# Optimization experiments

Measured on AMD Instinct MI355X. Metric: run time of the kernel, lower is better.

The kernel has to match this reference:

```python
import jax, jax.numpy as jnp
import numpy as np

B, W, V, D, H = 8, 1024, 512, 1024, 8
DK = D // H
SCALE = 1.0 / float(np.sqrt(DK))
EPS = 1e-5


def ln(x, g, b):
    m = x.mean(-1, keepdims=True)
    v = ((x - m) ** 2).mean(-1, keepdims=True)
    return (x - m) * jax.lax.rsqrt(v + EPS) * g + b


def setup_inputs() -> dict:
    key = jax.random.key(0)
    ks = iter(jax.random.split(key, 32))

    def wmat(shape):
        return jax.random.normal(next(ks), shape, jnp.float32) * 0.02

    inp = {
        'x': jax.random.normal(next(ks), (B, W, D), jnp.float32),
        'y': jax.random.normal(next(ks), (B, V, D), jnp.float32),
        'mask': jnp.ones((B, 1, W, W), jnp.bool_),
        # res1 pre-norm
        'ln_r1_g': jnp.ones((D,), jnp.float32), 'ln_r1_b': jnp.zeros((D,), jnp.float32),
        # self-attention projections (stored [in,out])
        'sa_wq': wmat((D, D)), 'sa_bq': jnp.zeros((D,), jnp.float32),
        'sa_wk': wmat((D, D)), 'sa_bk': jnp.zeros((D,), jnp.float32),
        'sa_wv': wmat((D, D)), 'sa_bv': jnp.zeros((D,), jnp.float32),
        'sa_wo': wmat((D, D)), 'sa_bo': jnp.zeros((D,), jnp.float32),
        # cross-attention norms + projections
        'ca_tn_g': jnp.ones((D,), jnp.float32), 'ca_tn_b': jnp.zeros((D,), jnp.float32),
        'ca_an_g': jnp.ones((D,), jnp.float32), 'ca_an_b': jnp.zeros((D,), jnp.float32),
        'ca_wq': wmat((D, D)), 'ca_bq': jnp.zeros((D,), jnp.float32),
        'ca_wk': wmat((D, D)), 'ca_bk': jnp.zeros((D,), jnp.float32),
        'ca_wv': wmat((D, D)), 'ca_bv': jnp.zeros((D,), jnp.float32),
        # post-cross norms
        'n1_g': jnp.ones((D,), jnp.float32), 'n1_b': jnp.zeros((D,), jnp.float32),
        'n2_g': jnp.ones((D,), jnp.float32), 'n2_b': jnp.zeros((D,), jnp.float32),
        # res2 pre-norm + FFN (hidden = 2*D per UniDecoderLayer)
        'ln_r2_g': jnp.ones((D,), jnp.float32), 'ln_r2_b': jnp.zeros((D,), jnp.float32),
        'ff_w1': wmat((D, 2 * D)), 'ff_b1': jnp.zeros((2 * D,), jnp.float32),
        'ff_w2': wmat((2 * D, D)), 'ff_b2': jnp.zeros((D,), jnp.float32),
    }
    return inp


def reference(x, y, mask,
              ln_r1_g, ln_r1_b,
              sa_wq, sa_bq, sa_wk, sa_bk, sa_wv, sa_bv, sa_wo, sa_bo,
              ca_tn_g, ca_tn_b, ca_an_g, ca_an_b,
              ca_wq, ca_bq, ca_wk, ca_bk, ca_wv, ca_bv,
              n1_g, n1_b, n2_g, n2_b,
              ln_r2_g, ln_r2_b, ff_w1, ff_b1, ff_w2, ff_b2):
    # --- res1: x + self_attn(LN(x)) (dropout p=0) ---
    h = ln(x, ln_r1_g, ln_r1_b)
    q = (h @ sa_wq + sa_bq).reshape(B, W, H, DK)
    k = (h @ sa_wk + sa_bk).reshape(B, W, H, DK)
    v = (h @ sa_wv + sa_bv).reshape(B, W, H, DK)
    scores = jnp.einsum('bqhd,bkhd->bhqk', q, k) * SCALE
    scores = jnp.where(mask, scores, jnp.float32(-1e9))  # mask (B,1,W,W) broadcasts over heads
    a = jax.nn.softmax(scores, axis=-1)
    o = jnp.einsum('bhqk,bkhd->bqhd', a, v).reshape(B, W, D)
    x = x + (o @ sa_wo + sa_bo)

    # --- sigmoid-gated cross attention ---
    t = ln(x, ca_tn_g, ca_tn_b)
    av = ln(y, ca_an_g, ca_an_b)
    cq = (t @ ca_wq + ca_bq).reshape(B, W, H, DK)
    ck = (av @ ca_wk + ca_bk).reshape(B, V, H, DK)
    cv = (av @ ca_wv + ca_bv).reshape(B, V, H, DK)
    gate = jax.nn.sigmoid(jnp.einsum('bwhd,bvhd->bwvh', cq, ck) * SCALE)  # (B,W,V,H)
    res = jnp.einsum('bwvh,bvhd->bwhd', gate, cv).reshape(B, W, D)
    attn_out = gate.mean(-1)  # mean over heads -> (B,W,V)

    x = ln(x, n1_g, n1_b) + ln(res, n2_g, n2_b)

    # --- res2: x + FFN(LN(x)) ---
    h2 = ln(x, ln_r2_g, ln_r2_b)
    x = x + (jax.nn.relu(h2 @ ff_w1 + ff_b1) @ ff_w2 + ff_b2)
    return (x, attn_out)
```

## Files before the change

kernel.cpp:

```cpp
#include <hip/hip_runtime.h>


typedef __bf16 bf16;
typedef bf16  bf16x4 __attribute__((ext_vector_type(4)));
typedef bf16  bf16x8 __attribute__((ext_vector_type(8)));
typedef float f32x4  __attribute__((ext_vector_type(4)));

#define SCALE 0.08838834764831845f

__device__ __forceinline__ f32x4 mfma16(bf16x8 a, bf16x8 b, f32x4 c) {
  return __builtin_amdgcn_mfma_f32_16x16x32_bf16(a, b, c, 0, 0, 0);
}

__device__ __forceinline__ void gll16(const bf16* g, bf16* l) {
  __builtin_amdgcn_global_load_lds(
      (__attribute__((address_space(1))) void*)(void*)g,
      (__attribute__((address_space(3))) void*)(void*)l, 16, 0, 0);
}

__device__ __forceinline__ void xcd_tile(int& bm, int& bn) {
  const int nx = gridDim.x;
  const int nwg = nx * gridDim.y;
  int bid = blockIdx.y * nx + blockIdx.x;
  const int cpx = nwg >> 3;
  bid = (bid & 7) * cpx + (bid >> 3);
  bn = (bid % nx) * 128;
  bm = (bid / nx) * 128;
}

__global__ __launch_bounds__(256) void gemm_bt(
    const bf16* __restrict__ A, const bf16* __restrict__ Bt,
    const float* __restrict__ bias,
    const bf16* __restrict__ residB, const float* __restrict__ residF,
    bf16* __restrict__ Cb, float* __restrict__ Cf,
    int M, int N, int K, int relu)
{
  __shared__ alignas(16) bf16 As[128 * 32];
  __shared__ alignas(16) bf16 Bs[128 * 32];
  const int tid  = threadIdx.x;
  const int wid  = tid >> 6;
  const int lane = tid & 63;
  const int l15  = lane & 15;
  const int quad = lane >> 4;
  int bm, bn;
  xcd_tile(bm, bn);
  const int wm = (wid & 1) * 64,  wn = (wid >> 1) * 64;

  f32x4 acc[4][4] = {};

  const int srow = tid >> 2;
  const int scol = (tid & 3) * 8;
  const bf16* ag0 = A  + (long)(bm + srow) * K + scol;
  const bf16* ag1 = ag0 + (long)64 * K;
  const bf16* bg0 = Bt + (long)(bn + srow) * K + scol;
  const bf16* bg1 = bg0 + (long)64 * K;
  bf16* lA0 = As + wid * 512;
  bf16* lA1 = As + 2048 + wid * 512;
  bf16* lB0 = Bs + wid * 512;
  bf16* lB1 = Bs + 2048 + wid * 512;

  for (int k0 = 0; k0 < K; k0 += 32) {
    gll16(ag0 + k0, lA0);
    gll16(ag1 + k0, lA1);
    gll16(bg0 + k0, lB0);
    gll16(bg1 + k0, lB1);
    __syncthreads();
    bf16x8 af[4], bfr[4];
#pragma unroll
    for (int i = 0; i < 4; ++i)
      af[i] = *(const bf16x8*)(As + (wm + i * 16 + l15) * 32 + quad * 8);
#pragma unroll
    for (int i = 0; i < 4; ++i)
      bfr[i] = *(const bf16x8*)(Bs + (wn + i * 16 + l15) * 32 + quad * 8);
#pragma unroll
    for (int mt = 0; mt < 4; ++mt)
#pragma unroll
      for (int nt = 0; nt < 4; ++nt)
        acc[mt][nt] = mfma16(af[mt], bfr[nt], acc[mt][nt]);
    __syncthreads();
  }

#pragma unroll
  for (int nt = 0; nt < 4; ++nt) {
    const int col = bn + wn + nt * 16 + l15;
    const float bv = bias ? bias[col] : 0.f;
#pragma unroll
    for (int mt = 0; mt < 4; ++mt) {
      const int row0 = bm + wm + mt * 16 + quad * 4;
#pragma unroll
      for (int r = 0; r < 4; ++r) {
        const long idx = (long)(row0 + r) * N + col;
        float v = acc[mt][nt][r] + bv;
        if (relu) v = fmaxf(v, 0.f);
        if (residB) v += (float)residB[idx];
        if (residF) v += residF[idx];
        if (Cb) Cb[idx] = (bf16)v;
        if (Cf) Cf[idx] = v;
      }
    }
  }
}

struct Out3 {
  bf16* o0; bf16* o1; bf16* o2;
  const float* b0; const float* b1; const float* b2;
};

__global__ __launch_bounds__(256) void gemm_bt_split(
    const bf16* __restrict__ A, const bf16* __restrict__ Bt,
    Out3 so, int M, int Ntot, int K)
{
  __shared__ alignas(16) bf16 As[128 * 32];
  __shared__ alignas(16) bf16 Bs[128 * 32];
  const int tid  = threadIdx.x;
  const int wid  = tid >> 6;
  const int lane = tid & 63;
  const int l15  = lane & 15;
  const int quad = lane >> 4;
  int bm, bn;
  xcd_tile(bm, bn);
  const int wm = (wid & 1) * 64,  wn = (wid >> 1) * 64;

  const int ch = bn >> 10;
  bf16* C = (ch == 0) ? so.o0 : (ch == 1 ? so.o1 : so.o2);
  const float* bp = (ch == 0) ? so.b0 : (ch == 1 ? so.b1 : so.b2);

  f32x4 acc[4][4] = {};

  const int srow = tid >> 2;
  const int scol = (tid & 3) * 8;
  const bf16* ag0 = A  + (long)(bm + srow) * K + scol;
  const bf16* ag1 = ag0 + (long)64 * K;
  const bf16* bg0 = Bt + (long)(bn + srow) * K + scol;
  const bf16* bg1 = bg0 + (long)64 * K;
  bf16* lA0 = As + wid * 512;
  bf16* lA1 = As + 2048 + wid * 512;
  bf16* lB0 = Bs + wid * 512;
  bf16* lB1 = Bs + 2048 + wid * 512;

  for (int k0 = 0; k0 < K; k0 += 32) {
    gll16(ag0 + k0, lA0);
    gll16(ag1 + k0, lA1);
    gll16(bg0 + k0, lB0);
    gll16(bg1 + k0, lB1);
    __syncthreads();
    bf16x8 af[4], bfr[4];
#pragma unroll
    for (int i = 0; i < 4; ++i)
      af[i] = *(const bf16x8*)(As + (wm + i * 16 + l15) * 32 + quad * 8);
#pragma unroll
    for (int i = 0; i < 4; ++i)
      bfr[i] = *(const bf16x8*)(Bs + (wn + i * 16 + l15) * 32 + quad * 8);
#pragma unroll
    for (int mt = 0; mt < 4; ++mt)
#pragma unroll
      for (int nt = 0; nt < 4; ++nt)
        acc[mt][nt] = mfma16(af[mt], bfr[nt], acc[mt][nt]);
    __syncthreads();
  }

#pragma unroll
  for (int nt = 0; nt < 4; ++nt) {
    const int col = bn + wn + nt * 16 + l15;
    const int cc  = col & 1023;
    const float bv = bp[cc];
#pragma unroll
    for (int mt = 0; mt < 4; ++mt) {
      const int row0 = bm + wm + mt * 16 + quad * 4;
#pragma unroll
      for (int r = 0; r < 4; ++r)
        C[(long)(row0 + r) * 1024 + cc] = (bf16)(acc[mt][nt][r] + bv);
    }
  }
  (void)M; (void)Ntot;
}

__global__ __launch_bounds__(512) void attn_self(
    const bf16* __restrict__ Q, const bf16* __restrict__ Km,
    const bf16* __restrict__ Vt, bf16* __restrict__ O)
{
  __shared__ alignas(16) bf16 Ks[16384];
  __shared__ alignas(16) bf16 Vs[16384];
  __shared__ alignas(16) bf16 Ps[8192];
  const int tid  = threadIdx.x;
  const int wid  = tid >> 6;
  const int lane = tid & 63;
  const int l15  = lane & 15;
  const int quad = lane >> 4;
  const int b = blockIdx.y >> 3, h = blockIdx.y & 7;
  const int q0 = blockIdx.x * 128;

  const int rdoff = l15 * 32 + (((quad ^ ((l15 >> 1) & 3))) << 3);

  const long qb = ((long)(b * 1024 + q0 + wid * 16 + l15)) * 1024 + h * 128 + quad * 8;
  bf16x8 qf[4];
#pragma unroll
  for (int ks = 0; ks < 4; ++ks) qf[ks] = *(const bf16x8*)(Q + qb + ks * 32);

  f32x4 oacc[8] = {};
  float mrow[4], lrow[4];
#pragma unroll
  for (int r = 0; r < 4; ++r) { mrow[r] = -3.0e38f; lrow[r] = 0.f; }

  const long kbase = (long)(b * 1024) * 1024 + h * 128;
  const long vbase = (long)(b * 8 + h) * 128 * 1024;

  const int srow = tid >> 3;
  const int sc8  = (tid & 7) * 8;

  bf16* pw = Ps + wid * 1024;

  for (int t = 0; t < 8; ++t) {
    const int kv0 = t * 128;
    __syncthreads();
#pragma unroll
    for (int dh = 0; dh < 2; ++dh)
#pragma unroll
      for (int kq = 0; kq < 2; ++kq) {
        const int kv = kq * 64 + srow;
        const int d  = dh * 64 + sc8;
        bf16x8 v = *(const bf16x8*)(Km + kbase + (long)(kv0 + kv) * 1024 + d);
        *(bf16x8*)(Ks + (d >> 5) * 4096 + kv * 32 +
                   (((((d & 31) >> 3) ^ ((kv >> 1) & 3))) << 3)) = v;
      }
#pragma unroll
    for (int kh = 0; kh < 2; ++kh)
#pragma unroll
      for (int dq = 0; dq < 2; ++dq) {
        const int d  = dq * 64 + srow;
        const int kv = kh * 64 + sc8;
        bf16x8 v = *(const bf16x8*)(Vt + vbase + (long)d * 1024 + kv0 + kv);
        *(bf16x8*)(Vs + (kv >> 5) * 4096 + d * 32 +
                   (((((kv & 31) >> 3) ^ ((d >> 1) & 3))) << 3)) = v;
      }
    __syncthreads();

    f32x4 sacc[8] = {};
#pragma unroll
    for (int nt = 0; nt < 8; ++nt)
#pragma unroll
      for (int ks = 0; ks < 4; ++ks)
        sacc[nt] = mfma16(qf[ks],
            *(const bf16x8*)(Ks + ks * 4096 + nt * 512 + rdoff),
            sacc[nt]);

    float tm[4];
#pragma unroll
    for (int r = 0; r < 4; ++r) {
      float m = -3.0e38f;
#pragma unroll
      for (int nt = 0; nt < 8; ++nt) m = fmaxf(m, sacc[nt][r]);
      tm[r] = m * SCALE;
    }
#pragma unroll
    for (int off = 8; off; off >>= 1)
#pragma unroll
      for (int r = 0; r < 4; ++r) tm[r] = fmaxf(tm[r], __shfl_xor(tm[r], off));
    float alpha[4], psum[4];
#pragma unroll
    for (int r = 0; r < 4; ++r) {
      const float mnew = fmaxf(mrow[r], tm[r]);
      alpha[r] = __expf(mrow[r] - mnew);
      mrow[r] = mnew;
      psum[r] = 0.f;
    }
#pragma unroll
    for (int nt = 0; nt < 8; ++nt)
#pragma unroll
      for (int r = 0; r < 4; ++r) oacc[nt][r] *= alpha[r];

#pragma unroll
    for (int hs = 0; hs < 2; ++hs) {
#pragma unroll
      for (int n2 = 0; n2 < 4; ++n2) {
        const int nt = hs * 4 + n2;
#pragma unroll
        for (int r = 0; r < 4; ++r) {
          const float p = __expf(sacc[nt][r] * SCALE - mrow[r]);
          psum[r] += p;
          const int prow = quad * 4 + r;
          pw[((nt >> 1) & 1) * 512 + prow * 32 +
             (((((nt & 1) * 2 + (l15 >> 3)) ^ ((prow >> 1) & 3))) << 3) + (l15 & 7)] =
              (bf16)p;
        }
      }
#pragma unroll
      for (int ks2 = 0; ks2 < 2; ++ks2) {
        const bf16x8 pa = *(const bf16x8*)(pw + ks2 * 512 + rdoff);
        const int ksx = hs * 2 + ks2;
#pragma unroll
        for (int nt = 0; nt < 8; ++nt)
          oacc[nt] = mfma16(pa,
              *(const bf16x8*)(Vs + ksx * 4096 + nt * 512 + rdoff),
              oacc[nt]);
      }
    }

#pragma unroll
    for (int off = 8; off; off >>= 1)
#pragma unroll
      for (int r = 0; r < 4; ++r) psum[r] += __shfl_xor(psum[r], off);
#pragma unroll
    for (int r = 0; r < 4; ++r) lrow[r] = lrow[r] * alpha[r] + psum[r];
  }

  float linv[4];
#pragma unroll
  for (int r = 0; r < 4; ++r) linv[r] = 1.f / lrow[r];
#pragma unroll
  for (int nt = 0; nt < 8; ++nt)
#pragma unroll
    for (int r = 0; r < 4; ++r) {
      const int row = q0 + wid * 16 + quad * 4 + r;
      O[((long)(b * 1024 + row)) * 1024 + h * 128 + nt * 16 + l15] =
          (bf16)(oacc[nt][r] * linv[r]);
    }
}

__global__ __launch_bounds__(256) void gate2(
    const bf16* __restrict__ CQ, const bf16* __restrict__ CK,
    bf16* __restrict__ gA, bf16* __restrict__ gB)
{
  __shared__ alignas(16) bf16 Ks[16384];
  __shared__ alignas(16) bf16 Pt[4][1024];
  const int tid  = threadIdx.x;
  const int wid  = tid >> 6;
  const int lane = tid & 63;
  const int l15  = lane & 15;
  const int quad = lane >> 4;
  const int z = blockIdx.y, b = z >> 3, h = z & 7;
  const int w0 = blockIdx.x * 32;
  const int rsel = wid & 1, vsel = wid >> 1;

  const int rdoff = l15 * 32 + (((quad ^ ((l15 >> 1) & 3))) << 3);

  bf16* Gz = (z < 32) ? (gA + (long)z * 524288) : (gB + (long)(z - 32) * 524288);

  const long qb = ((long)(b * 1024 + w0 + rsel * 16 + l15)) * 1024 + h * 128 + quad * 8;
  bf16x8 qf[4];
#pragma unroll
  for (int ks = 0; ks < 4; ++ks) qf[ks] = *(const bf16x8*)(CQ + qb + ks * 32);

  const int srow = tid >> 3;
  const int sc8  = (tid & 7) * 8;

  for (int vt = 0; vt < 4; ++vt) {
    const int v0 = vt * 128;
    __syncthreads();
#pragma unroll
    for (int i = 0; i < 4; ++i) {
      const int v = i * 32 + srow;
#pragma unroll
      for (int dh = 0; dh < 2; ++dh) {
        const int d = dh * 64 + sc8;
        bf16x8 val = *(const bf16x8*)(CK + ((long)(b * 512 + v0 + v)) * 1024 + h * 128 + d);
        *(bf16x8*)(Ks + (d >> 5) * 4096 + v * 32 +
                   (((((d & 31) >> 3) ^ ((v >> 1) & 3))) << 3)) = val;
      }
    }
    __syncthreads();

    f32x4 sacc[4] = {};
#pragma unroll
    for (int nt = 0; nt < 4; ++nt)
#pragma unroll
      for (int ks = 0; ks < 4; ++ks)
        sacc[nt] = mfma16(qf[ks],
            *(const bf16x8*)(Ks + ks * 4096 + vsel * 2048 + nt * 512 + rdoff),
            sacc[nt]);

#pragma unroll
    for (int nt = 0; nt < 4; ++nt)
#pragma unroll
      for (int r = 0; r < 4; ++r) {
        const float g = 1.f / (1.f + __expf(-sacc[nt][r] * SCALE));
        const int prow = quad * 4 + r;
        const int g0 = nt * 2 + (l15 >> 3);
        Pt[wid][prow * 64 + ((g0 ^ ((prow >> 1) & 3)) << 3) + (l15 & 7)] = (bf16)g;
      }
#pragma unroll
    for (int pass = 0; pass < 2; ++pass) {
      const int f = pass * 512 + lane * 8;
      const int row = f >> 6, col = f & 63;
      const int gl = (lane & 7) ^ ((row >> 1) & 3);
      bf16x8 vv = *(const bf16x8*)(&Pt[wid][row * 64 + gl * 8]);
      *(bf16x8*)(Gz + (long)(w0 + rsel * 16 + row) * 512 + v0 + vsel * 64 + col) = vv;
    }
  }
}

__global__ __launch_bounds__(256) void reduce_h(
    const bf16* __restrict__ gA, const bf16* __restrict__ gB,
    float* __restrict__ AOUT)
{
  const int idx = blockIdx.x * 256 + threadIdx.x;
  const int v4 = idx & 127;
  const int w  = (idx >> 7) & 1023;
  const int b  = idx >> 17;
  float s0 = 0.f, s1 = 0.f, s2 = 0.f, s3 = 0.f;
#pragma unroll
  for (int h = 0; h < 8; ++h) {
    const int z = b * 8 + h;
    const bf16* base = (z < 32) ? (gA + (long)z * 524288) : (gB + (long)(z - 32) * 524288);
    bf16x4 g = *(const bf16x4*)(base + (long)w * 512 + v4 * 4);
    s0 += (float)g[0]; s1 += (float)g[1]; s2 += (float)g[2]; s3 += (float)g[3];
  }
  *(float4*)(AOUT + (long)idx * 4) =
      make_float4(s0 * 0.125f, s1 * 0.125f, s2 * 0.125f, s3 * 0.125f);
}

__global__ __launch_bounds__(256) void gemm_res(
    const bf16* __restrict__ gA, const bf16* __restrict__ gB,
    const bf16* __restrict__ CVt, bf16* __restrict__ RES)
{
  __shared__ alignas(16) bf16 As[128 * 32];
  __shared__ alignas(16) bf16 Bs[128 * 32];
  const int tid  = threadIdx.x;
  const int wid  = tid >> 6;
  const int lane = tid & 63;
  const int l15  = lane & 15;
  const int quad = lane >> 4;
  const int z = blockIdx.z, b = z >> 3, h = z & 7;
  const bf16* A  = (z < 32) ? (gA + (long)z * 524288) : (gB + (long)(z - 32) * 524288);
  const bf16* Bt = CVt + (long)z * 65536;
  const int bm = blockIdx.x * 128;
  const int wm = (wid & 1) * 64, wn = (wid >> 1) * 64;

  f32x4 acc[4][4] = {};

  const int srow = tid >> 2;
  const int scol = (tid & 3) * 8;
  const bf16* ag0 = A  + (long)(bm + srow) * 512 + scol;
  const bf16* ag1 = ag0 + (long)64 * 512;
  const bf16* bg0 = Bt + (long)srow * 512 + scol;
  const bf16* bg1 = bg0 + (long)64 * 512;
  bf16* lA0 = As + wid * 512;
  bf16* lA1 = As + 2048 + wid * 512;
  bf16* lB0 = Bs + wid * 512;
  bf16* lB1 = Bs + 2048 + wid * 512;

  for (int k0 = 0; k0 < 512; k0 += 32) {
    gll16(ag0 + k0, lA0);
    gll16(ag1 + k0, lA1);
    gll16(bg0 + k0, lB0);
    gll16(bg1 + k0, lB1);
    __syncthreads();
    bf16x8 af[4], bfr[4];
#pragma unroll
    for (int i = 0; i < 4; ++i)
      af[i] = *(const bf16x8*)(As + (wm + i * 16 + l15) * 32 + quad * 8);
#pragma unroll
    for (int i = 0; i < 4; ++i)
      bfr[i] = *(const bf16x8*)(Bs + (wn + i * 16 + l15) * 32 + quad * 8);
#pragma unroll
    for (int mt = 0; mt < 4; ++mt)
#pragma unroll
      for (int nt = 0; nt < 4; ++nt)
        acc[mt][nt] = mfma16(af[mt], bfr[nt], acc[mt][nt]);
    __syncthreads();
  }

#pragma unroll
  for (int nt = 0; nt < 4; ++nt) {
    const int col = h * 128 + wn + nt * 16 + l15;
#pragma unroll
    for (int mt = 0; mt < 4; ++mt) {
      const int row0 = bm + wm + mt * 16 + quad * 4;
#pragma unroll
      for (int r = 0; r < 4; ++r)
        RES[((long)(b * 1024 + row0 + r)) * 1024 + col] = (bf16)acc[mt][nt][r];
    }
  }
}

template <typename T>
__global__ __launch_bounds__(256) void transpose_k(
    const T* __restrict__ in, bf16* __restrict__ out,
    int sIR, int sOR, long inStrideB, long inStrideH, long outStrideZ, int H)
{
  __shared__ bf16 t[32][33];
  const int z = blockIdx.z;
  const T* ib = in + (long)(z / H) * inStrideB + (long)(z % H) * inStrideH;
  bf16* ob = out + (long)z * outStrideZ;
  const int r0 = blockIdx.x * 32, c0 = blockIdx.y * 32;
  const int tx = threadIdx.x & 31, ty = threadIdx.x >> 5;
#pragma unroll
  for (int i = 0; i < 32; i += 8)
    t[ty + i][tx] = (bf16)(float)ib[(long)(r0 + ty + i) * sIR + (c0 + tx)];
  __syncthreads();
#pragma unroll
  for (int i = 0; i < 32; i += 8)
    ob[(long)(c0 + ty + i) * sOR + (r0 + tx)] = t[tx][ty + i];
}

struct TP9 { const float* in[9]; bf16* out[9]; };

__global__ __launch_bounds__(256) void transpose_w9(TP9 p)
{
  __shared__ bf16 t[32][33];
  const int z = blockIdx.z;
  int r0, c0, sIR, sOR;
  if (z < 7) {
    if (blockIdx.y >= 32) return;
    r0 = blockIdx.x * 32; c0 = blockIdx.y * 32; sIR = 1024; sOR = 1024;
  } else if (z == 7) {
    r0 = blockIdx.x * 32; c0 = blockIdx.y * 32; sIR = 2048; sOR = 1024;
  } else {
    r0 = blockIdx.y * 32; c0 = blockIdx.x * 32; sIR = 1024; sOR = 2048;
  }
  const float* ib = p.in[z];
  bf16* ob = p.out[z];
  const int tx = threadIdx.x & 31, ty = threadIdx.x >> 5;
#pragma unroll
  for (int i = 0; i < 32; i += 8)
    t[ty + i][tx] = (bf16)ib[(long)(r0 + ty + i) * sIR + (c0 + tx)];
  __syncthreads();
#pragma unroll
  for (int i = 0; i < 32; i += 8)
    ob[(long)(c0 + ty + i) * sOR + (r0 + tx)] = t[tx][ty + i];
}

__device__ __forceinline__ void load16v(float* d, const bf16* p) {
  bf16x8 a = *(const bf16x8*)p, b2 = *(const bf16x8*)(p + 8);
#pragma unroll
  for (int j = 0; j < 8; ++j) { d[j] = (float)a[j]; d[j + 8] = (float)b2[j]; }
}
__device__ __forceinline__ void load16v(float* d, const float* p) {
#pragma unroll
  for (int j = 0; j < 4; ++j) {
    float4 v = ((const float4*)p)[j];
    d[4*j] = v.x; d[4*j+1] = v.y; d[4*j+2] = v.z; d[4*j+3] = v.w;
  }
}

template <typename TI>
__device__ __forceinline__ void ln_row_body(
    const TI* __restrict__ X, const float* __restrict__ G,
    const float* __restrict__ Bb, bf16* __restrict__ out, long row, int lane)
{
  const int c0 = lane * 16;
  const long base = row * 1024 + c0;
  float a[16];
  load16v(a, X + base);
  float s = 0.f, ss = 0.f;
#pragma unroll
  for (int j = 0; j < 16; ++j) { s += a[j]; ss += a[j] * a[j]; }
#pragma unroll
  for (int off = 32; off; off >>= 1) { s += __shfl_xor(s, off); ss += __shfl_xor(ss, off); }
  const float inv = 1.f / 1024.f;
  const float m = s * inv;
  const float rr = rsqrtf(fmaxf(ss * inv - m * m, 0.f) + 1e-5f);
  bf16x8 o0, o1;
#pragma unroll
  for (int j = 0; j < 16; ++j) {
    float v = (a[j] - m) * rr * G[c0 + j] + Bb[c0 + j];
    if (j < 8) o0[j] = (bf16)v; else o1[j - 8] = (bf16)v;
  }
  *(bf16x8*)(out + base) = o0;
  *(bf16x8*)(out + base + 8) = o1;
}

template <typename TI>
__global__ __launch_bounds__(256) void ln_k(
    const TI* __restrict__ X, const float* __restrict__ G1,
    const float* __restrict__ B1, bf16* __restrict__ out)
{
  const int wid = threadIdx.x >> 6, lane = threadIdx.x & 63;
  ln_row_body<TI>(X, G1, B1, out, (long)blockIdx.x * 4 + wid, lane);
}

__global__ __launch_bounds__(256) void ln_pair(
    const bf16* __restrict__ Xa, const float* __restrict__ Ga,
    const float* __restrict__ Ba, bf16* __restrict__ outA,
    const float* __restrict__ Xb, const float* __restrict__ Gb,
    const float* __restrict__ Bb, bf16* __restrict__ outB)
{
  const int wid = threadIdx.x >> 6, lane = threadIdx.x & 63;
  const long row = (long)blockIdx.x * 4 + wid;
  if (blockIdx.x < 2048) ln_row_body<bf16>(Xa, Ga, Ba, outA, row, lane);
  else                   ln_row_body<float>(Xb, Gb, Bb, outB, row - 8192, lane);
}

__global__ __launch_bounds__(256) void ln_fuse2(
    const bf16* __restrict__ X1, const float* __restrict__ G1, const float* __restrict__ B1,
    const bf16* __restrict__ X2, const float* __restrict__ G2, const float* __restrict__ B2,
    const float* __restrict__ G3, const float* __restrict__ B3,
    bf16* __restrict__ outX, bf16* __restrict__ outH)
{
  const int wid = threadIdx.x >> 6, lane = threadIdx.x & 63;
  const long row = (long)blockIdx.x * 4 + wid;
  const int c0 = lane * 16;
  const long base = row * 1024 + c0;

  float a[16], b[16];
  load16v(a, X1 + base);
  load16v(b, X2 + base);
  float s1 = 0.f, ss1 = 0.f, s2 = 0.f, ss2 = 0.f;
#pragma unroll
  for (int j = 0; j < 16; ++j) {
    s1 += a[j]; ss1 += a[j] * a[j];
    s2 += b[j]; ss2 += b[j] * b[j];
  }
#pragma unroll
  for (int off = 32; off; off >>= 1) {
    s1 += __shfl_xor(s1, off); ss1 += __shfl_xor(ss1, off);
    s2 += __shfl_xor(s2, off); ss2 += __shfl_xor(ss2, off);
  }
  const float inv = 1.f / 1024.f;
  const float m1 = s1 * inv;
  const float r1 = rsqrtf(fmaxf(ss1 * inv - m1 * m1, 0.f) + 1e-5f);
  const float m2 = s2 * inv;
  const float r2 = rsqrtf(fmaxf(ss2 * inv - m2 * m2, 0.f) + 1e-5f);

  float v[16];
  float s3 = 0.f, ss3 = 0.f;
  bf16x8 o0, o1;
#pragma unroll
  for (int j = 0; j < 16; ++j) {
    v[j] = (a[j] - m1) * r1 * G1[c0 + j] + B1[c0 + j]
         + (b[j] - m2) * r2 * G2[c0 + j] + B2[c0 + j];
    s3 += v[j]; ss3 += v[j] * v[j];
    if (j < 8) o0[j] = (bf16)v[j]; else o1[j - 8] = (bf16)v[j];
  }
  *(bf16x8*)(outX + base) = o0;
  *(bf16x8*)(outX + base + 8) = o1;
#pragma unroll
  for (int off = 32; off; off >>= 1) {
    s3 += __shfl_xor(s3, off); ss3 += __shfl_xor(ss3, off);
  }
  const float m3 = s3 * inv;
  const float r3 = rsqrtf(fmaxf(ss3 * inv - m3 * m3, 0.f) + 1e-5f);
#pragma unroll
  for (int j = 0; j < 16; ++j) {
    float hh = (v[j] - m3) * r3 * G3[c0 + j] + B3[c0 + j];
    if (j < 8) o0[j] = (bf16)hh; else o1[j - 8] = (bf16)hh;
  }
  *(bf16x8*)(outH + base) = o0;
  *(bf16x8*)(outH + base + 8) = o1;
}

extern "C" void kernel_launch(void* const* d_in, const int* in_sizes, int n_in,
                              void* d_out, int out_size, void* d_ws, size_t ws_size,
                              hipStream_t stream) {
  (void)in_sizes; (void)n_in; (void)out_size; (void)ws_size;

  const float* x   = (const float*)d_in[0];
  const float* y   = (const float*)d_in[1];
  const float* r1g = (const float*)d_in[3];  const float* r1b = (const float*)d_in[4];
  const float* sa_wq = (const float*)d_in[5];  const float* sa_bq = (const float*)d_in[6];
  const float* sa_wk = (const float*)d_in[7];  const float* sa_bk = (const float*)d_in[8];
  const float* sa_wv = (const float*)d_in[9];  const float* sa_bv = (const float*)d_in[10];
  const float* sa_wo = (const float*)d_in[11]; const float* sa_bo = (const float*)d_in[12];
  const float* tn_g = (const float*)d_in[13];  const float* tn_b = (const float*)d_in[14];
  const float* an_g = (const float*)d_in[15];  const float* an_b = (const float*)d_in[16];
  const float* ca_wq = (const float*)d_in[17]; const float* ca_bq = (const float*)d_in[18];
  const float* ca_wk = (const float*)d_in[19]; const float* ca_bk = (const float*)d_in[20];
  const float* ca_wv = (const float*)d_in[21];
  const float* ca_bv = (const float*)d_in[22];
  const float* n1g = (const float*)d_in[23];   const float* n1b = (const float*)d_in[24];
  const float* n2g = (const float*)d_in[25];   const float* n2b = (const float*)d_in[26];
  const float* r2g = (const float*)d_in[27];   const float* r2b = (const float*)d_in[28];
  const float* fw1 = (const float*)d_in[29];   const float* fb1 = (const float*)d_in[30];
  const float* fw2 = (const float*)d_in[31];   const float* fb2 = (const float*)d_in[32];

  char* wsb = (char*)d_ws;
  const size_t MBy = 1048576;
  bf16* fw1T = (bf16*)(wsb + 0 * MBy);
  bf16* fw2T = (bf16*)(wsb + 4 * MBy);
  bf16* wqT  = (bf16*)(wsb + 8 * MBy);
  bf16* wkT  = (bf16*)(wsb + 10 * MBy);
  bf16* wvT  = (bf16*)(wsb + 12 * MBy);
  bf16* woT  = (bf16*)(wsb + 14 * MBy);
  bf16* cwqT = (bf16*)(wsb + 16 * MBy);
  bf16* cwkT = (bf16*)(wsb + 18 * MBy);
  bf16* cwvT = (bf16*)(wsb + 20 * MBy);
  bf16* h_bf = (bf16*)(wsb + 22 * MBy);
  bf16* t_bf = h_bf;  bf16* h2_bf = h_bf;
  bf16* q_bf = (bf16*)(wsb + 38 * MBy);
  bf16* av_bf = q_bf;
  bf16* gA = (bf16*)(wsb + 22 * MBy);
  bf16* k_bf = (bf16*)(wsb + 54 * MBy);
  bf16* cq_bf = k_bf;  bf16* res_b = k_bf;
  bf16* v_bf = (bf16*)(wsb + 70 * MBy);
  bf16* ck_bf = v_bf;
  bf16* cv_bf = (bf16*)(wsb + 78 * MBy);
  bf16* x2_b  = v_bf;
  bf16* vT  = (bf16*)(wsb + 86 * MBy);
  bf16* cvT = vT;
  bf16* o_bf = (bf16*)(wsb + 102 * MBy);
  bf16* x1_b = o_bf;
  bf16* gB  = (bf16*)(wsb + 118 * MBy);
  bf16* ffh = gB;

  float* out_x    = (float*)d_out;
  float* out_attn = out_x + 8 * 1024 * 1024;

  const dim3 blk(256);

  TP9 tp;
  tp.in[0] = sa_wq; tp.out[0] = wqT;
  tp.in[1] = sa_wk; tp.out[1] = wkT;
  tp.in[2] = sa_wv; tp.out[2] = wvT;
  tp.in[3] = sa_wo; tp.out[3] = woT;
  tp.in[4] = ca_wq; tp.out[4] = cwqT;
  tp.in[5] = ca_wk; tp.out[5] = cwkT;
  tp.in[6] = ca_wv; tp.out[6] = cwvT;
  tp.in[7] = fw1;   tp.out[7] = fw1T;
  tp.in[8] = fw2;   tp.out[8] = fw2T;
  transpose_w9<<<dim3(32, 64, 9), blk, 0, stream>>>(tp);

  ln_k<float><<<dim3(2048), blk, 0, stream>>>(x, r1g, r1b, h_bf);

  Out3 oqkv = { q_bf, k_bf, v_bf, sa_bq, sa_bk, sa_bv };
  gemm_bt_split<<<dim3(24, 64), blk, 0, stream>>>(h_bf, wqT, oqkv, 8192, 3072, 1024);

  transpose_k<bf16><<<dim3(32, 4, 64), blk, 0, stream>>>(v_bf, vT, 1024, 1024,
      (long)1024 * 1024, 128, (long)128 * 1024, 8);

  attn_self<<<dim3(8, 64), dim3(512), 0, stream>>>(q_bf, k_bf, vT, o_bf);

  gemm_bt<<<dim3(8, 64), blk, 0, stream>>>(o_bf, woT, sa_bo, nullptr, x, x1_b, nullptr, 8192, 1024, 1024, 0);

  ln_pair<<<dim3(3072), blk, 0, stream>>>(x1_b, tn_g, tn_b, t_bf, y, an_g, an_b, av_bf);

  gemm_bt<<<dim3(8, 64), blk, 0, stream>>>(t_bf, cwqT, ca_bq, nullptr, nullptr, cq_bf, nullptr, 8192, 1024, 1024, 0);

  Out3 ockv = { ck_bf, cv_bf, nullptr, ca_bk, ca_bv, nullptr };
  gemm_bt_split<<<dim3(16, 32), blk, 0, stream>>>(av_bf, cwkT, ockv, 4096, 2048, 1024);

  transpose_k<bf16><<<dim3(16, 4, 64), blk, 0, stream>>>(cv_bf, cvT, 1024, 512,
      (long)512 * 1024, 128, (long)128 * 512, 8);

  gate2<<<dim3(32, 64), blk, 0, stream>>>(cq_bf, ck_bf, gA, gB);
  reduce_h<<<dim3(4096), blk, 0, stream>>>(gA, gB, out_attn);
  gemm_res<<<dim3(8, 1, 64), blk, 0, stream>>>(gA, gB, cvT, res_b);

  ln_fuse2<<<dim3(2048), blk, 0, stream>>>(x1_b, n1g, n1b, res_b, n2g, n2b,
                                           r2g, r2b, x2_b, h2_bf);

  gemm_bt<<<dim3(16, 64), blk, 0, stream>>>(h2_bf, fw1T, fb1, nullptr, nullptr, ffh, nullptr, 8192, 2048, 1024, 1);
  gemm_bt<<<dim3(8, 64), blk, 0, stream>>>(ffh, fw2T, fb2, x2_b, nullptr, nullptr, out_x, 8192, 1024, 2048, 0);
}
```

Baseline: 699.4 us.

## Double GEMM K-step to 64 and merge cross-attn projections and reduce/res launches

All bf16 GEMM kernels now stage a 64-wide K slice per iteration, two 32-wide halves in LDS, halving the number of barrier pairs per tile. The cross-attention Q projection and the K/V projections are fused into one split-GEMM launch that selects its A operand per output chunk, with blocks past the shorter M range exiting early. The head-mean reduction and the gate·V GEMM are merged into a single launch that dispatches on block index. The cost is doubled LDS per block, which may lower occupancy.

```diff
diff --git a/kernel.cpp b/kernel.cpp
--- a/kernel.cpp
+++ b/kernel.cpp
@@ -35,8 +35,8 @@
     bf16* __restrict__ Cb, float* __restrict__ Cf,
     int M, int N, int K, int relu)
 {
-  __shared__ alignas(16) bf16 As[128 * 32];
-  __shared__ alignas(16) bf16 Bs[128 * 32];
+  __shared__ alignas(16) bf16 As[128 * 64];
+  __shared__ alignas(16) bf16 Bs[128 * 64];
   const int tid  = threadIdx.x;
   const int wid  = tid >> 6;
   const int lane = tid & 63;
@@ -56,27 +56,38 @@
   const bf16* bg1 = bg0 + (long)64 * K;
   bf16* lA0 = As + wid * 512;
   bf16* lA1 = As + 2048 + wid * 512;
+  bf16* lA2 = As + 4096 + wid * 512;
+  bf16* lA3 = As + 6144 + wid * 512;
   bf16* lB0 = Bs + wid * 512;
   bf16* lB1 = Bs + 2048 + wid * 512;
-
-  for (int k0 = 0; k0 < K; k0 += 32) {
+  bf16* lB2 = Bs + 4096 + wid * 512;
+  bf16* lB3 = Bs + 6144 + wid * 512;
+
+  for (int k0 = 0; k0 < K; k0 += 64) {
     gll16(ag0 + k0, lA0);
     gll16(ag1 + k0, lA1);
+    gll16(ag0 + k0 + 32, lA2);
+    gll16(ag1 + k0 + 32, lA3);
     gll16(bg0 + k0, lB0);
     gll16(bg1 + k0, lB1);
-    __syncthreads();
-    bf16x8 af[4], bfr[4];
-#pragma unroll
-    for (int i = 0; i < 4; ++i)
-      af[i] = *(const bf16x8*)(As + (wm + i * 16 + l15) * 32 + quad * 8);
-#pragma unroll
-    for (int i = 0; i < 4; ++i)
-      bfr[i] = *(const bf16x8*)(Bs + (wn + i * 16 + l15) * 32 + quad * 8);
-#pragma unroll
-    for (int mt = 0; mt < 4; ++mt)
-#pragma unroll
-      for (int nt = 0; nt < 4; ++nt)
-        acc[mt][nt] = mfma16(af[mt], bfr[nt], acc[mt][nt]);
+    gll16(bg0 + k0 + 32, lB2);
+    gll16(bg1 + k0 + 32, lB3);
+    __syncthreads();
+#pragma unroll
+    for (int kk = 0; kk < 2; ++kk) {
+      bf16x8 af[4], bfr[4];
+#pragma unroll
+      for (int i = 0; i < 4; ++i)
+        af[i] = *(const bf16x8*)(As + kk * 4096 + (wm + i * 16 + l15) * 32 + quad * 8);
+#pragma unroll
+      for (int i = 0; i < 4; ++i)
+        bfr[i] = *(const bf16x8*)(Bs + kk * 4096 + (wn + i * 16 + l15) * 32 + quad * 8);
+#pragma unroll
+      for (int mt = 0; mt < 4; ++mt)
+#pragma unroll
+        for (int nt = 0; nt < 4; ++nt)
+          acc[mt][nt] = mfma16(af[mt], bfr[nt], acc[mt][nt]);
+    }
     __syncthreads();
   }
 
@@ -107,11 +118,11 @@
 };
 
 __global__ __launch_bounds__(256) void gemm_bt_split(
-    const bf16* __restrict__ A, const bf16* __restrict__ Bt,
-    Out3 so, int M, int Ntot, int K)
-{
-  __shared__ alignas(16) bf16 As[128 * 32];
-  __shared__ alignas(16) bf16 Bs[128 * 32];
+    const bf16* __restrict__ A0, const bf16* __restrict__ A1,
+    const bf16* __restrict__ Bt, Out3 so, int m1lim, int K)
+{
+  __shared__ alignas(16) bf16 As[128 * 64];
+  __shared__ alignas(16) bf16 Bs[128 * 64];
   const int tid  = threadIdx.x;
   const int wid  = tid >> 6;
   const int lane = tid & 63;
@@ -122,6 +133,8 @@
   const int wm = (wid & 1) * 64,  wn = (wid >> 1) * 64;
 
   const int ch = bn >> 10;
+  if (ch > 0 && bm >= m1lim) return;
+  const bf16* A = (ch == 0) ? A0 : A1;
   bf16* C = (ch == 0) ? so.o0 : (ch == 1 ? so.o1 : so.o2);
   const float* bp = (ch == 0) ? so.b0 : (ch == 1 ? so.b1 : so.b2);
 
@@ -135,27 +148,38 @@
   const bf16* bg1 = bg0 + (long)64 * K;
   bf16* lA0 = As + wid * 512;
   bf16* lA1 = As + 2048 + wid * 512;
+  bf16* lA2 = As + 4096 + wid * 512;
+  bf16* lA3 = As + 6144 + wid * 512;
   bf16* lB0 = Bs + wid * 512;
   bf16* lB1 = Bs + 2048 + wid * 512;
-
-  for (int k0 = 0; k0 < K; k0 += 32) {
+  bf16* lB2 = Bs + 4096 + wid * 512;
+  bf16* lB3 = Bs + 6144 + wid * 512;
+
+  for (int k0 = 0; k0 < K; k0 += 64) {
     gll16(ag0 + k0, lA0);
     gll16(ag1 + k0, lA1);
+    gll16(ag0 + k0 + 32, lA2);
+    gll16(ag1 + k0 + 32, lA3);
     gll16(bg0 + k0, lB0);
     gll16(bg1 + k0, lB1);
-    __syncthreads();
-    bf16x8 af[4], bfr[4];
-#pragma unroll
-    for (int i = 0; i < 4; ++i)
-      af[i] = *(const bf16x8*)(As + (wm + i * 16 + l15) * 32 + quad * 8);
-#pragma unroll
-    for (int i = 0; i < 4; ++i)
-      bfr[i] = *(const bf16x8*)(Bs + (wn + i * 16 + l15) * 32 + quad * 8);
-#pragma unroll
-    for (int mt = 0; mt < 4; ++mt)
-#pragma unroll
-      for (int nt = 0; nt < 4; ++nt)
-        acc[mt][nt] = mfma16(af[mt], bfr[nt], acc[mt][nt]);
+    gll16(bg0 + k0 + 32, lB2);
+    gll16(bg1 + k0 + 32, lB3);
+    __syncthreads();
+#pragma unroll
+    for (int kk = 0; kk < 2; ++kk) {
+      bf16x8 af[4], bfr[4];
+#pragma unroll
+      for (int i = 0; i < 4; ++i)
+        af[i] = *(const bf16x8*)(As + kk * 4096 + (wm + i * 16 + l15) * 32 + quad * 8);
+#pragma unroll
+      for (int i = 0; i < 4; ++i)
+        bfr[i] = *(const bf16x8*)(Bs + kk * 4096 + (wn + i * 16 + l15) * 32 + quad * 8);
+#pragma unroll
+      for (int mt = 0; mt < 4; ++mt)
+#pragma unroll
+        for (int nt = 0; nt < 4; ++nt)
+          acc[mt][nt] = mfma16(af[mt], bfr[nt], acc[mt][nt]);
+    }
     __syncthreads();
   }
 
@@ -172,7 +196,6 @@
         C[(long)(row0 + r) * 1024 + cc] = (bf16)(acc[mt][nt][r] + bv);
     }
   }
-  (void)M; (void)Ntot;
 }
 
 __global__ __launch_bounds__(512) void attn_self(
@@ -389,41 +412,43 @@
   }
 }
 
-__global__ __launch_bounds__(256) void reduce_h(
+__global__ __launch_bounds__(256) void reduce_res(
     const bf16* __restrict__ gA, const bf16* __restrict__ gB,
-    float* __restrict__ AOUT)
-{
-  const int idx = blockIdx.x * 256 + threadIdx.x;
-  const int v4 = idx & 127;
-  const int w  = (idx >> 7) & 1023;
-  const int b  = idx >> 17;
-  float s0 = 0.f, s1 = 0.f, s2 = 0.f, s3 = 0.f;
-#pragma unroll
-  for (int h = 0; h < 8; ++h) {
-    const int z = b * 8 + h;
-    const bf16* base = (z < 32) ? (gA + (long)z * 524288) : (gB + (long)(z - 32) * 524288);
-    bf16x4 g = *(const bf16x4*)(base + (long)w * 512 + v4 * 4);
-    s0 += (float)g[0]; s1 += (float)g[1]; s2 += (float)g[2]; s3 += (float)g[3];
-  }
-  *(float4*)(AOUT + (long)idx * 4) =
-      make_float4(s0 * 0.125f, s1 * 0.125f, s2 * 0.125f, s3 * 0.125f);
-}
-
-__global__ __launch_bounds__(256) void gemm_res(
-    const bf16* __restrict__ gA, const bf16* __restrict__ gB,
-    const bf16* __restrict__ CVt, bf16* __restrict__ RES)
-{
-  __shared__ alignas(16) bf16 As[128 * 32];
-  __shared__ alignas(16) bf16 Bs[128 * 32];
-  const int tid  = threadIdx.x;
+    const bf16* __restrict__ CVt, float* __restrict__ AOUT,
+    bf16* __restrict__ RES)
+{
+  __shared__ alignas(16) bf16 As[128 * 64];
+  __shared__ alignas(16) bf16 Bs[128 * 64];
+  const int bid = blockIdx.x;
+  const int tid = threadIdx.x;
+
+  if (bid < 4096) {
+    const int idx = bid * 256 + tid;
+    const int v4 = idx & 127;
+    const int w  = (idx >> 7) & 1023;
+    const int b  = idx >> 17;
+    float s0 = 0.f, s1 = 0.f, s2 = 0.f, s3 = 0.f;
+#pragma unroll
+    for (int h = 0; h < 8; ++h) {
+      const int z = b * 8 + h;
+      const bf16* base = (z < 32) ? (gA + (long)z * 524288) : (gB + (long)(z - 32) * 524288);
+      bf16x4 g = *(const bf16x4*)(base + (long)w * 512 + v4 * 4);
+      s0 += (float)g[0]; s1 += (float)g[1]; s2 += (float)g[2]; s3 += (float)g[3];
+    }
+    *(float4*)(AOUT + (long)idx * 4) =
+        make_float4(s0 * 0.125f, s1 * 0.125f, s2 * 0.125f, s3 * 0.125f);
+    return;
+  }
+
+  const int bid2 = bid - 4096;
+  const int z = bid2 >> 3, b = z >> 3, h = z & 7;
+  const int bm = (bid2 & 7) * 128;
   const int wid  = tid >> 6;
   const int lane = tid & 63;
   const int l15  = lane & 15;
   const int quad = lane >> 4;
-  const int z = blockIdx.z, b = z >> 3, h = z & 7;
   const bf16* A  = (z < 32) ? (gA + (long)z * 524288) : (gB + (long)(z - 32) * 524288);
   const bf16* Bt = CVt + (long)z * 65536;
-  const int bm = blockIdx.x * 128;
   const int wm = (wid & 1) * 64, wn = (wid >> 1) * 64;
 
   f32x4 acc[4][4] = {};
@@ -436,27 +461,38 @@
   const bf16* bg1 = bg0 + (long)64 * 512;
   bf16* lA0 = As + wid * 512;
   bf16* lA1 = As + 2048 + wid * 512;
+  bf16* lA2 = As + 4096 + wid * 512;
+  bf16* lA3 = As + 6144 + wid * 512;
   bf16* lB0 = Bs + wid * 512;
   bf16* lB1 = Bs + 2048 + wid * 512;
-
-  for (int k0 = 0; k0 < 512; k0 += 32) {
+  bf16* lB2 = Bs + 4096 + wid * 512;
+  bf16* lB3 = Bs + 6144 + wid * 512;
+
+  for (int k0 = 0; k0 < 512; k0 += 64) {
     gll16(ag0 + k0, lA0);
     gll16(ag1 + k0, lA1);
+    gll16(ag0 + k0 + 32, lA2);
+    gll16(ag1 + k0 + 32, lA3);
     gll16(bg0 + k0, lB0);
     gll16(bg1 + k0, lB1);
-    __syncthreads();
-    bf16x8 af[4], bfr[4];
-#pragma unroll
-    for (int i = 0; i < 4; ++i)
-      af[i] = *(const bf16x8*)(As + (wm + i * 16 + l15) * 32 + quad * 8);
-#pragma unroll
-    for (int i = 0; i < 4; ++i)
-      bfr[i] = *(const bf16x8*)(Bs + (wn + i * 16 + l15) * 32 + quad * 8);
-#pragma unroll
-    for (int mt = 0; mt < 4; ++mt)
-#pragma unroll
-      for (int nt = 0; nt < 4; ++nt)
-        acc[mt][nt] = mfma16(af[mt], bfr[nt], acc[mt][nt]);
+    gll16(bg0 + k0 + 32, lB2);
+    gll16(bg1 + k0 + 32, lB3);
+    __syncthreads();
+#pragma unroll
+    for (int kk = 0; kk < 2; ++kk) {
+      bf16x8 af[4], bfr[4];
+#pragma unroll
+      for (int i = 0; i < 4; ++i)
+        af[i] = *(const bf16x8*)(As + kk * 4096 + (wm + i * 16 + l15) * 32 + quad * 8);
+#pragma unroll
+      for (int i = 0; i < 4; ++i)
+        bfr[i] = *(const bf16x8*)(Bs + kk * 4096 + (wn + i * 16 + l15) * 32 + quad * 8);
+#pragma unroll
+      for (int mt = 0; mt < 4; ++mt)
+#pragma unroll
+        for (int nt = 0; nt < 4; ++nt)
+          acc[mt][nt] = mfma16(af[mt], bfr[nt], acc[mt][nt]);
+    }
     __syncthreads();
   }
 
@@ -712,7 +748,7 @@
   ln_k<float><<<dim3(2048), blk, 0, stream>>>(x, r1g, r1b, h_bf);
 
   Out3 oqkv = { q_bf, k_bf, v_bf, sa_bq, sa_bk, sa_bv };
-  gemm_bt_split<<<dim3(24, 64), blk, 0, stream>>>(h_bf, wqT, oqkv, 8192, 3072, 1024);
+  gemm_bt_split<<<dim3(24, 64), blk, 0, stream>>>(h_bf, h_bf, wqT, oqkv, 8192, 1024);
 
   transpose_k<bf16><<<dim3(32, 4, 64), blk, 0, stream>>>(v_bf, vT, 1024, 1024,
       (long)1024 * 1024, 128, (long)128 * 1024, 8);
@@ -723,17 +759,14 @@
 
   ln_pair<<<dim3(3072), blk, 0, stream>>>(x1_b, tn_g, tn_b, t_bf, y, an_g, an_b, av_bf);
 
-  gemm_bt<<<dim3(8, 64), blk, 0, stream>>>(t_bf, cwqT, ca_bq, nullptr, nullptr, cq_bf, nullptr, 8192, 1024, 1024, 0);
-
-  Out3 ockv = { ck_bf, cv_bf, nullptr, ca_bk, ca_bv, nullptr };
-  gemm_bt_split<<<dim3(16, 32), blk, 0, stream>>>(av_bf, cwkT, ockv, 4096, 2048, 1024);
+  Out3 ocq = { cq_bf, ck_bf, cv_bf, ca_bq, ca_bk, ca_bv };
+  gemm_bt_split<<<dim3(24, 64), blk, 0, stream>>>(t_bf, av_bf, cwqT, ocq, 4096, 1024);
 
   transpose_k<bf16><<<dim3(16, 4, 64), blk, 0, stream>>>(cv_bf, cvT, 1024, 512,
       (long)512 * 1024, 128, (long)128 * 512, 8);
 
   gate2<<<dim3(32, 64), blk, 0, stream>>>(cq_bf, ck_bf, gA, gB);
-  reduce_h<<<dim3(4096), blk, 0, stream>>>(gA, gB, out_attn);
-  gemm_res<<<dim3(8, 1, 64), blk, 0, stream>>>(gA, gB, cvT, res_b);
+  reduce_res<<<dim3(4608), blk, 0, stream>>>(gA, gB, cvT, out_attn, res_b);
 
   ln_fuse2<<<dim3(2048), blk, 0, stream>>>(x1_b, n1g, n1b, res_b, n2g, n2b,
                                            r2g, r2b, x2_b, h2_bf);
```

Measured after the change: 666.1 us. -4.8%, faster.
